# Performance work log

Measured on AMD Instinct MI355X. Metric: run time of the kernel, lower is better.

## Reference

```python
import math
import jax, jax.numpy as jnp
import numpy as np

B, T, G, E, H, L = 8, 32, 32, 768, 12, 4
S = T * G
HD = E // H


def setup_inputs() -> dict:
    key = jax.random.key(0)
    ks = jax.random.split(key, 10)
    def n(k, shape, s=0.02):
        return s * jax.random.normal(k, shape, jnp.float32)
    return dict(
        x=jax.random.normal(ks[0], (B, T, G, E), jnp.float32),
        study_date=jnp.sort(jax.random.randint(ks[1], (B, T), 0, 50), axis=-1),
        wpe=n(ks[2], (50, E)),
        ln1_w=jnp.ones((L, E)), ln1_b=jnp.zeros((L, E)),
        in_w=n(ks[3], (L, 3 * E, E)), in_b=jnp.zeros((L, 3 * E)),
        out_w=n(ks[4], (L, E, E)), out_b=jnp.zeros((L, E)),
        ln2_w=jnp.ones((L, E)), ln2_b=jnp.zeros((L, E)),
        fc_w=n(ks[5], (L, 4 * E, E)), fc_b=jnp.zeros((L, 4 * E)),
        proj_w=n(ks[6], (L, E, 4 * E), 0.02 / math.sqrt(2 * L)),
        proj_b=jnp.zeros((L, E)),
        lnf_w=jnp.ones((E,)), lnf_b=jnp.zeros((E,)),
    )


def _ln(x, w, b):
    m = x.mean(-1, keepdims=True)
    v = ((x - m) ** 2).mean(-1, keepdims=True)
    return (x - m) / jnp.sqrt(v + 1e-5) * w + b


def _gelu_new(x):
    # NewGELU: 0.5*x*(1+tanh(sqrt(2/pi)*(x+0.044715*x^3)))
    c = np.sqrt(2.0 / np.pi).astype(np.float32)
    return 0.5 * x * (1.0 + jnp.tanh(c * (x + 0.044715 * x ** 3)))


def _mask_bias():
    # block-causal mask: tril over T blocks, each expanded to G x G
    allowed = jnp.tril(jnp.ones((T, T), bool))
    allowed = jnp.repeat(jnp.repeat(allowed, G, axis=0), G, axis=1)  # [S,S]
    return jnp.where(allowed, 0.0, -jnp.inf).astype(jnp.float32)


def reference(x, study_date, wpe, ln1_w, ln1_b, in_w, in_b, out_w, out_b,
              ln2_w, ln2_b, fc_w, fc_b, proj_w, proj_b, lnf_w, lnf_b):
    b, t, g, d = x.shape
    s = t * g
    pos = wpe[jnp.clip(study_date, 0, 49)]  # [B,T,E]
    pos = jnp.broadcast_to(pos[:, :, None, :], (b, t, g, d)).reshape(b, s, d)
    h = x.reshape(b, s, d) + pos
    bias = _mask_bias()  # [S,S]
    inv_sqrt_hd = 1.0 / np.sqrt(HD).astype(np.float32)
    for l in range(L):
        y = _ln(h, ln1_w[l], ln1_b[l])
        qkv = y @ in_w[l].T + in_b[l]  # [B,S,3E]
        q, k, v = jnp.split(qkv, 3, axis=-1)
        q = q.reshape(b, s, H, HD).transpose(0, 2, 1, 3)
        k = k.reshape(b, s, H, HD).transpose(0, 2, 1, 3)
        v = v.reshape(b, s, H, HD).transpose(0, 2, 1, 3)
        att = jnp.einsum('bhqd,bhkd->bhqk', q, k) * inv_sqrt_hd + bias
        att = jax.nn.softmax(att, axis=-1)
        o = jnp.einsum('bhqk,bhkd->bhqd', att, v)
        o = o.transpose(0, 2, 1, 3).reshape(b, s, d)
        h = h + o @ out_w[l].T + out_b[l]
        y2 = _ln(h, ln2_w[l], ln2_b[l])
        h = h + _gelu_new(y2 @ fc_w[l].T + fc_b[l]) @ proj_w[l].T + proj_b[l]
    return _ln(h, lnf_w, lnf_b)
```

## Files before the change

### kernel.cpp

```cpp
#include <hip/hip_runtime.h>
#include <hip/hip_bf16.h>

typedef __attribute__((ext_vector_type(8))) __bf16 bf16x8;
typedef __attribute__((ext_vector_type(4))) float f32x4;

typedef unsigned short u16;

__device__ __forceinline__ u16 f2bf(float f) {
    unsigned int u = __float_as_uint(f);
    u += 0x7FFFu + ((u >> 16) & 1u);
    return (u16)(u >> 16);
}

__device__ __forceinline__ void g2l16(const void* g, void* l) {
    __builtin_amdgcn_global_load_lds(
        (const __attribute__((address_space(1))) void*)g,
        (__attribute__((address_space(3))) void*)l, 16, 0, 0);
}

#define BB 8
#define SS 1024
#define EE 768
#define HH 12
#define HD 64
#define LL 4

__global__ __launch_bounds__(256) void cvt_k(const float* __restrict__ in,
                                             u16* __restrict__ out, int n4) {
    for (int i = blockIdx.x * 256 + threadIdx.x; i < n4; i += gridDim.x * 256) {
        float4 v = ((const float4*)in)[i];
        ushort4 u;
        u.x = f2bf(v.x); u.y = f2bf(v.y); u.z = f2bf(v.z); u.w = f2bf(v.w);
        ((ushort4*)out)[i] = u;
    }
}

__global__ __launch_bounds__(256) void embed_k(const float* __restrict__ x,
                                               const int* __restrict__ sd,
                                               const float* __restrict__ wpe,
                                               float* __restrict__ h) {
    int idx = blockIdx.x * 256 + threadIdx.x;
    int e4 = idx % 192;
    int bs = idx / 192;
    int b = bs >> 10;
    int t = (bs >> 5) & 31;
    int date = sd[b * 32 + t];
    date = date < 0 ? 0 : (date > 49 ? 49 : date);
    float4 xv = ((const float4*)x)[idx];
    float4 pv = ((const float4*)wpe)[date * 192 + e4];
    float4 r; r.x = xv.x + pv.x; r.y = xv.y + pv.y; r.z = xv.z + pv.z; r.w = xv.w + pv.w;
    ((float4*)h)[idx] = r;
}

template <bool BF16OUT>
__global__ __launch_bounds__(256) void ln_k(const float* __restrict__ in,
                                            const float* __restrict__ w,
                                            const float* __restrict__ b,
                                            void* __restrict__ out) {
    int tid = threadIdx.x, wv = tid >> 6, lane = tid & 63;
    int token = blockIdx.x * 4 + wv;
    const float4* ip = (const float4*)(in + (size_t)token * EE);
    float4 v[3];
#pragma unroll
    for (int p = 0; p < 3; p++) v[p] = ip[p * 64 + lane];
    float s = 0.f;
#pragma unroll
    for (int p = 0; p < 3; p++) s += v[p].x + v[p].y + v[p].z + v[p].w;
#pragma unroll
    for (int m = 1; m < 64; m <<= 1) s += __shfl_xor(s, m);
    float mean = s * (1.f / 768.f);
    float vs = 0.f;
#pragma unroll
    for (int p = 0; p < 3; p++) {
        float dx = v[p].x - mean, dy = v[p].y - mean, dz = v[p].z - mean, dw = v[p].w - mean;
        vs += dx * dx + dy * dy + dz * dz + dw * dw;
    }
#pragma unroll
    for (int m = 1; m < 64; m <<= 1) vs += __shfl_xor(vs, m);
    float rstd = rsqrtf(vs * (1.f / 768.f) + 1e-5f);
    const float4* wp = (const float4*)w;
    const float4* bp = (const float4*)b;
#pragma unroll
    for (int p = 0; p < 3; p++) {
        float4 wv4 = wp[p * 64 + lane], bv4 = bp[p * 64 + lane];
        float rx = (v[p].x - mean) * rstd * wv4.x + bv4.x;
        float ry = (v[p].y - mean) * rstd * wv4.y + bv4.y;
        float rz = (v[p].z - mean) * rstd * wv4.z + bv4.z;
        float rw = (v[p].w - mean) * rstd * wv4.w + bv4.w;
        if (BF16OUT) {
            ushort4 u; u.x = f2bf(rx); u.y = f2bf(ry); u.z = f2bf(rz); u.w = f2bf(rw);
            ((ushort4*)((u16*)out + (size_t)token * EE))[p * 64 + lane] = u;
        } else {
            float4 r; r.x = rx; r.y = ry; r.z = rz; r.w = rw;
            ((float4*)((float*)out + (size_t)token * EE))[p * 64 + lane] = r;
        }
    }
}

template <int MODE, int BM>
__global__ __launch_bounds__(256) void gemm_bt(const u16* __restrict__ A,
                                               const u16* __restrict__ Bw,
                                               const float* __restrict__ bias,
                                               float* __restrict__ hres,
                                               u16* __restrict__ outb,
                                               u16* __restrict__ vT,
                                               u16* __restrict__ kT,
                                               int M, int N, int K) {
    constexpr int TM = BM / 32;
    constexpr int NST = (BM == 128) ? 3 : 4;
    constexpr int PD = NST - 2;
    constexpr int ATILE = BM * 32;
    constexpr int TILE = ATILE + 4096;
    constexpr int SSTR = TILE * 2;
    __shared__ u16 SM[NST * TILE];

    const int tid = threadIdx.x;
    const int lane = tid & 63, w = tid >> 6;
    const int quad = lane >> 4, l16 = lane & 15;

    const int nx = N >> 7;
    const int ny = M / BM;
    const int id = blockIdx.x;
    const int xcd = id & 7, s = id >> 3;
    const int yt = xcd * (ny >> 3) + s / nx;
    const int xt = s % nx;
    const int m0 = yt * BM, n0 = xt * 128;
    const int wm = (w >> 1) * (BM / 2), wn = (w & 1) * 64;

    f32x4 acc[TM][4];
#pragma unroll
    for (int i = 0; i < TM; i++)
#pragma unroll
        for (int j = 0; j < 4; j++) acc[i][j] = (f32x4){0.f, 0.f, 0.f, 0.f};

    const int swz = (quad ^ ((l16 >> 1) & 3)) * 8;
    const int nk = K >> 5;

    const int cB0 = w * 128 + lane, cB1 = cB0 + 64;
    const int rB0 = cB0 >> 2, gB0 = (((cB0 & 3) ^ ((cB0 >> 3) & 3)) * 8);
    const int rB1 = cB1 >> 2, gB1 = (((cB1 & 3) ^ ((cB1 >> 3) & 3)) * 8);
    const u16* Bp0 = Bw + (size_t)(n0 + rB0) * K + gB0;
    const u16* Bp1 = Bw + (size_t)(n0 + rB1) * K + gB1;
    char* lB0 = (char*)SM + ATILE * 2 + w * 2048;
    char* lB1 = lB0 + 1024;
    const int cA0 = (BM == 128) ? cB0 : tid;
    const int rA0 = cA0 >> 2, gA0 = (((cA0 & 3) ^ ((cA0 >> 3) & 3)) * 8);
    const u16* Ap0 = A + (size_t)(m0 + rA0) * K + gA0;
    char* lA0 = (char*)SM + ((BM == 128) ? w * 2048 : w * 1024);
    const int cA1 = cB1;
    const int rA1 = cA1 >> 2, gA1 = (((cA1 & 3) ^ ((cA1 >> 3) & 3)) * 8);
    const u16* Ap1 = A + (size_t)(m0 + rA1) * K + gA1;
    char* lA1 = (char*)SM + w * 2048 + 1024;

    g2l16(Ap0, lA0);
    if (BM == 128) g2l16(Ap1, lA1);
    g2l16(Bp0, lB0);
    g2l16(Bp1, lB1);
    if (PD == 2) {
        g2l16(Ap0 + 32, lA0 + SSTR);
        if (BM == 128) g2l16(Ap1 + 32, lA1 + SSTR);
        g2l16(Bp0 + 32, lB0 + SSTR);
        g2l16(Bp1 + 32, lB1 + SSTR);
    }

    int rb = 0, wb = PD;
    for (int ki = 0; ki < nk; ki++) {
        if (ki + PD < nk) {
            const int kb = (ki + PD) << 5;
            const int bo = wb * SSTR;
            g2l16(Ap0 + kb, lA0 + bo);
            if (BM == 128) g2l16(Ap1 + kb, lA1 + bo);
            g2l16(Bp0 + kb, lB0 + bo);
            g2l16(Bp1 + kb, lB1 + bo);
        }
        if (BM == 128) {
            if (ki < nk - 1) __builtin_amdgcn_s_waitcnt(0x0F74);
            else             __builtin_amdgcn_s_waitcnt(0x0F70);
        } else {
            if (ki < nk - 2)      __builtin_amdgcn_s_waitcnt(0x0F76);
            else if (ki == nk - 2) __builtin_amdgcn_s_waitcnt(0x0F73);
            else                  __builtin_amdgcn_s_waitcnt(0x0F70);
        }
        __builtin_amdgcn_s_barrier();

        const u16* Ab = (const u16*)SM + rb * TILE;
        const u16* Bb = Ab + ATILE;
        bf16x8 af[TM], bfr[4];
#pragma unroll
        for (int t = 0; t < TM; t++)
            af[t] = *(const bf16x8*)(Ab + (wm + t * 16 + l16) * 32 + swz);
#pragma unroll
        for (int t = 0; t < 4; t++)
            bfr[t] = *(const bf16x8*)(Bb + (wn + t * 16 + l16) * 32 + swz);
#pragma unroll
        for (int tm = 0; tm < TM; tm++)
#pragma unroll
            for (int tn = 0; tn < 4; tn++)
                acc[tm][tn] = __builtin_amdgcn_mfma_f32_16x16x32_bf16(
                    af[tm], bfr[tn], acc[tm][tn], 0, 0, 0);
        rb = (rb + 1 == NST) ? 0 : rb + 1;
        wb = (wb + 1 == NST) ? 0 : wb + 1;
    }

#pragma unroll
    for (int tm = 0; tm < TM; tm++) {
        int rowm = m0 + wm + tm * 16 + quad * 4;
#pragma unroll
        for (int tn = 0; tn < 4; tn++) {
            int coln = n0 + wn + tn * 16 + l16;
            float bv = bias[coln];
            f32x4 v = acc[tm][tn];
            if (MODE == 0) {
                int b = rowm >> 10, s2 = rowm & 1023;
                if (coln < EE) {
                    int hh = coln >> 6, d = coln & 63;
                    u16* qp = outb + ((size_t)(b * HH + hh) * SS + s2) * HD + d;
#pragma unroll
                    for (int r = 0; r < 4; r++) qp[r * HD] = f2bf(v[r] + bv);
                } else if (coln < 2 * EE) {
                    int hh = (coln - EE) >> 6, d = (coln - EE) & 63;
                    u16* kp = kT + ((size_t)(b * HH + hh) * SS + s2) * HD + d;
#pragma unroll
                    for (int r = 0; r < 4; r++) kp[r * HD] = f2bf(v[r] + bv);
                } else {
                    int hh = (coln - 2 * EE) >> 6, d = (coln - 2 * EE) & 63;
                    ushort4 pk;
                    pk.x = f2bf(v[0] + bv); pk.y = f2bf(v[1] + bv);
                    pk.z = f2bf(v[2] + bv); pk.w = f2bf(v[3] + bv);
                    *(ushort4*)(vT + (((size_t)((b * HH + hh) * HD + d)) << 10) + s2) = pk;
                }
            } else if (MODE == 1) {
#pragma unroll
                for (int r = 0; r < 4; r++) {
                    size_t idx = (size_t)(rowm + r) * N + coln;
                    hres[idx] += v[r] + bv;
                }
            } else {
#pragma unroll
                for (int r = 0; r < 4; r++) {
                    float x = v[r] + bv;
                    float t = x + 0.044715f * x * x * x;
                    float e = __expf(-1.5957691216057308f * t);
                    float th = (1.f - e) / (1.f + e);
                    outb[(size_t)(rowm + r) * N + coln] = f2bf(0.5f * x * (1.f + th));
                }
            }
        }
    }
}

__global__ __launch_bounds__(256) void attn_k(const u16* __restrict__ qT,
                                              const u16* __restrict__ kT,
                                              const u16* __restrict__ vT,
                                              u16* __restrict__ o) {
    __shared__ u16 Ks[2048];
    __shared__ u16 Vs[2048];
    __shared__ u16 P[4][16 * 40];
    int tid = threadIdx.x, w = tid >> 6, lane = tid & 63;
    int quad = lane >> 4, l16 = lane & 15;
    int blk = blockIdx.x;
    int qg = 15 - (blk / 96);
    int bh = blk % 96;
    int b = bh / HH, hh = bh % HH;
    int q0 = qg * 64;
    int kend_blk = q0 + 64;
    int kend_w = q0 + ((w >> 1) ? 64 : 32);

    const u16* qbase = qT + ((size_t)bh * SS + q0 + w * 16 + l16) * HD + quad * 8;
    bf16x8 qf0 = *(const bf16x8*)(qbase);
    bf16x8 qf1 = *(const bf16x8*)(qbase + 32);

    f32x4 of[4];
#pragma unroll
    for (int i = 0; i < 4; i++) of[i] = (f32x4){0.f, 0.f, 0.f, 0.f};
    float mrun[4], lrun[4];
#pragma unroll
    for (int r = 0; r < 4; r++) { mrun[r] = -__builtin_inff(); lrun[r] = 0.f; }

    int tK = tid >> 3, dcK = ((tid & 7) ^ (tK & 7));
    const u16* kg = kT + ((size_t)bh * SS + tK) * HD + dcK * 8;
    char* kl = (char*)Ks + w * 1024;
    int dV = tid >> 2, tcV = ((tid & 3) ^ ((dV >> 1) & 3));
    const u16* vg = vT + ((size_t)bh * HD + dV) * SS + tcV * 8;
    char* vl = (char*)Vs + w * 1024;
    u16* Pw = P[w];

    for (int kb = 0; kb < kend_blk; kb += 32) {
        g2l16(kg + (size_t)kb * HD, kl);
        g2l16(vg + kb, vl);
        __syncthreads();
        if (kb < kend_w) {
            int t0 = l16, t1 = 16 + l16;
            bf16x8 k00 = *(const bf16x8*)(Ks + (t0 * 8 + (quad ^ (l16 & 7))) * 8);
            bf16x8 k01 = *(const bf16x8*)(Ks + (t0 * 8 + ((4 + quad) ^ (l16 & 7))) * 8);
            bf16x8 k10 = *(const bf16x8*)(Ks + (t1 * 8 + (quad ^ (l16 & 7))) * 8);
            bf16x8 k11 = *(const bf16x8*)(Ks + (t1 * 8 + ((4 + quad) ^ (l16 & 7))) * 8);
            f32x4 s0 = (f32x4){0.f, 0.f, 0.f, 0.f};
            f32x4 s1 = (f32x4){0.f, 0.f, 0.f, 0.f};
            s0 = __builtin_amdgcn_mfma_f32_16x16x32_bf16(qf0, k00, s0, 0, 0, 0);
            s0 = __builtin_amdgcn_mfma_f32_16x16x32_bf16(qf1, k01, s0, 0, 0, 0);
            s1 = __builtin_amdgcn_mfma_f32_16x16x32_bf16(qf0, k10, s1, 0, 0, 0);
            s1 = __builtin_amdgcn_mfma_f32_16x16x32_bf16(qf1, k11, s1, 0, 0, 0);

            float alpha[4];
#pragma unroll
            for (int r = 0; r < 4; r++) {
                float a0 = s0[r] * 0.125f, a1 = s1[r] * 0.125f;
                float mx = fmaxf(a0, a1);
#pragma unroll
                for (int m = 1; m < 16; m <<= 1) mx = fmaxf(mx, __shfl_xor(mx, m));
                float mnew = fmaxf(mrun[r], mx);
                alpha[r] = __expf(mrun[r] - mnew);
                float p0 = __expf(a0 - mnew);
                float p1 = __expf(a1 - mnew);
                float ps = p0 + p1;
#pragma unroll
                for (int m = 1; m < 16; m <<= 1) ps += __shfl_xor(ps, m);
                lrun[r] = lrun[r] * alpha[r] + ps;
                mrun[r] = mnew;
                Pw[(quad * 4 + r) * 40 + l16] = f2bf(p0);
                Pw[(quad * 4 + r) * 40 + 16 + l16] = f2bf(p1);
            }
#pragma unroll
            for (int n4 = 0; n4 < 4; n4++) {
                of[n4][0] *= alpha[0]; of[n4][1] *= alpha[1];
                of[n4][2] *= alpha[2]; of[n4][3] *= alpha[3];
            }
            bf16x8 pf = *(const bf16x8*)(Pw + l16 * 40 + quad * 8);
#pragma unroll
            for (int n4 = 0; n4 < 4; n4++) {
                int d = n4 * 16 + l16;
                bf16x8 vf = *(const bf16x8*)(Vs + (d * 4 + (quad ^ ((d >> 1) & 3))) * 8);
                of[n4] = __builtin_amdgcn_mfma_f32_16x16x32_bf16(pf, vf, of[n4], 0, 0, 0);
            }
        }
        __syncthreads();
    }

    float inv[4];
#pragma unroll
    for (int r = 0; r < 4; r++) inv[r] = 1.f / lrun[r];
#pragma unroll
    for (int n4 = 0; n4 < 4; n4++)
#pragma unroll
        for (int r = 0; r < 4; r++)
            o[(size_t)(b * SS + q0 + w * 16 + quad * 4 + r) * EE + hh * HD + n4 * 16 + l16] =
                f2bf(of[n4][r] * inv[r]);
}

extern "C" void kernel_launch(void* const* d_in, const int* in_sizes, int n_in,
                              void* d_out, int out_size, void* d_ws, size_t ws_size,
                              hipStream_t stream) {
    const float* x     = (const float*)d_in[0];
    const int*   sd    = (const int*)d_in[1];
    const float* wpe   = (const float*)d_in[2];
    const float* ln1w  = (const float*)d_in[3];
    const float* ln1b  = (const float*)d_in[4];
    const float* in_w  = (const float*)d_in[5];
    const float* in_b  = (const float*)d_in[6];
    const float* out_w = (const float*)d_in[7];
    const float* out_b = (const float*)d_in[8];
    const float* ln2w  = (const float*)d_in[9];
    const float* ln2b  = (const float*)d_in[10];
    const float* fc_w  = (const float*)d_in[11];
    const float* fc_b  = (const float*)d_in[12];
    const float* pr_w  = (const float*)d_in[13];
    const float* pr_b  = (const float*)d_in[14];
    const float* lnfw  = (const float*)d_in[15];
    const float* lnfb  = (const float*)d_in[16];
    float* outp = (float*)d_out;

    char* ws = (char*)d_ws;
    float* h   = (float*)ws;
    u16* ybuf  = (u16*)(ws + 25165824);
    u16* big   = (u16*)(ws + 37748736);
    u16* qT    = big;
    u16* kT    = big + 6291456;
    u16* vT    = (u16*)(ws + 88080384);
    u16* wb    = (u16*)(ws + 100663296);
    u16* w_in  = wb;
    u16* w_out = w_in + 7077888;
    u16* w_fc  = w_out + 2359296;
    u16* w_pr  = w_fc + 9437184;

    cvt_k<<<1024, 256, 0, stream>>>(in_w,  w_in,  7077888 / 4);
    cvt_k<<<1024, 256, 0, stream>>>(out_w, w_out, 2359296 / 4);
    cvt_k<<<1024, 256, 0, stream>>>(fc_w,  w_fc,  9437184 / 4);
    cvt_k<<<1024, 256, 0, stream>>>(pr_w,  w_pr,  9437184 / 4);
    embed_k<<<6144, 256, 0, stream>>>(x, sd, wpe, h);

    for (int l = 0; l < LL; l++) {
        ln_k<true><<<2048, 256, 0, stream>>>(h, ln1w + l * EE, ln1b + l * EE, ybuf);
        gemm_bt<0, 128><<<18 * 64, 256, 0, stream>>>(
            ybuf, w_in + (size_t)l * 2304 * 768, in_b + l * 2304, nullptr, qT, vT, kT,
            8192, 2304, 768);
        attn_k<<<1536, 256, 0, stream>>>(qT, kT, vT, ybuf);
        gemm_bt<1, 64><<<6 * 128, 256, 0, stream>>>(
            ybuf, w_out + (size_t)l * 768 * 768, out_b + l * 768, h, nullptr, nullptr, nullptr,
            8192, 768, 768);
        ln_k<true><<<2048, 256, 0, stream>>>(h, ln2w + l * EE, ln2b + l * EE, ybuf);
        gemm_bt<2, 128><<<24 * 64, 256, 0, stream>>>(
            ybuf, w_fc + (size_t)l * 3072 * 768, fc_b + l * 3072, nullptr, big, nullptr, nullptr,
            8192, 3072, 768);
        gemm_bt<1, 64><<<6 * 128, 256, 0, stream>>>(
            big, w_pr + (size_t)l * 768 * 3072, pr_b + l * 768, h, nullptr, nullptr, nullptr,
            8192, 768, 3072);
    }
    ln_k<false><<<2048, 256, 0, stream>>>(h, lnfw, lnfb, outp);
}
```

Measured before the change: 1.294 ms.

## Add register-staged B-operand GEMM for residual out-proj and MLP-proj

Adds a new GEMM kernel for the two residual-add projections. Only the A tile is staged through LDS, with a 4-stage ring and async global-to-LDS loads. Each wave loads its B (weight) fragments straight from global memory into a 3-deep register ring, with explicit vmcnt waits. This is meant to cut LDS traffic and bank pressure for the weight operand and to overlap loads with MFMA, at the cost of more registers and uncoalesced per-lane global loads of B. The kernel also uses XCD-aware block swizzling.

```diff
diff --git a/kernel.cpp b/kernel.cpp
--- a/kernel.cpp
+++ b/kernel.cpp
@@ -244,6 +244,104 @@
                     float th = (1.f - e) / (1.f + e);
                     outb[(size_t)(rowm + r) * N + coln] = f2bf(0.5f * x * (1.f + th));
                 }
+            }
+        }
+    }
+}
+
+__global__ __launch_bounds__(256, 3) void gemm_breg(const u16* __restrict__ A,
+                                                    const u16* __restrict__ Bw,
+                                                    const float* __restrict__ bias,
+                                                    float* __restrict__ hres,
+                                                    int M, int N, int K) {
+    constexpr int NST = 4;
+    __shared__ u16 SM[NST * 2048];
+
+    const int tid = threadIdx.x;
+    const int lane = tid & 63, w = tid >> 6;
+    const int quad = lane >> 4, l16 = lane & 15;
+
+    const int nx = N >> 7;
+    const int ny = M >> 6;
+    const int id = blockIdx.x;
+    const int xcd = id & 7, s = id >> 3;
+    const int yt = xcd * (ny >> 3) + s / nx;
+    const int xt = s % nx;
+    const int m0 = yt * 64, n0 = xt * 128;
+    const int wm = (w >> 1) * 32, wn = (w & 1) * 64;
+
+    f32x4 acc[2][4];
+#pragma unroll
+    for (int i = 0; i < 2; i++)
+#pragma unroll
+        for (int j = 0; j < 4; j++) acc[i][j] = (f32x4){0.f, 0.f, 0.f, 0.f};
+
+    const int swz = (quad ^ ((l16 >> 1) & 3)) * 8;
+    const int nk = K >> 5;
+
+    const int rA0 = tid >> 2, gA0 = (((tid & 3) ^ ((tid >> 3) & 3)) * 8);
+    const u16* Ap0 = A + (size_t)(m0 + rA0) * K + gA0;
+    char* lA0 = (char*)SM + w * 1024;
+
+    const u16* BpR[4];
+#pragma unroll
+    for (int t = 0; t < 4; t++)
+        BpR[t] = Bw + (size_t)(n0 + wn + t * 16 + l16) * K + quad * 8;
+
+    bf16x8 bb0[4], bb1[4], bb2[4];
+
+    g2l16(Ap0, lA0);
+#pragma unroll
+    for (int t = 0; t < 4; t++) bb0[t] = *(const bf16x8*)(BpR[t]);
+    g2l16(Ap0 + 32, lA0 + 4096);
+#pragma unroll
+    for (int t = 0; t < 4; t++) bb1[t] = *(const bf16x8*)(BpR[t] + 32);
+
+    int rb = 0;
+    for (int ki0 = 0; ki0 < nk; ki0 += 3) {
+#pragma unroll
+        for (int j = 0; j < 3; j++) {
+            const int ki = ki0 + j;
+            if (ki + 2 < nk) {
+                const int kb = (ki + 2) << 5;
+                g2l16(Ap0 + kb, lA0 + (size_t)((rb + 2) & 3) * 4096);
+                bf16x8* bw = (j == 0) ? bb2 : (j == 1) ? bb0 : bb1;
+#pragma unroll
+                for (int t = 0; t < 4; t++) bw[t] = *(const bf16x8*)(BpR[t] + kb);
+            }
+            const int rem = nk - 1 - ki;
+            if (rem >= 2)      asm volatile("s_waitcnt vmcnt(10)" ::: "memory");
+            else if (rem == 1) asm volatile("s_waitcnt vmcnt(5)" ::: "memory");
+            else               asm volatile("s_waitcnt vmcnt(0)" ::: "memory");
+            __builtin_amdgcn_s_barrier();
+
+            const u16* Ab = (const u16*)SM + rb * 2048;
+            bf16x8 af0 = *(const bf16x8*)(Ab + (wm + l16) * 32 + swz);
+            bf16x8 af1 = *(const bf16x8*)(Ab + (wm + 16 + l16) * 32 + swz);
+            const bf16x8* br = (j == 0) ? bb0 : (j == 1) ? bb1 : bb2;
+#pragma unroll
+            for (int tn = 0; tn < 4; tn++) {
+                acc[0][tn] = __builtin_amdgcn_mfma_f32_16x16x32_bf16(
+                    af0, br[tn], acc[0][tn], 0, 0, 0);
+                acc[1][tn] = __builtin_amdgcn_mfma_f32_16x16x32_bf16(
+                    af1, br[tn], acc[1][tn], 0, 0, 0);
+            }
+            rb = (rb + 1) & 3;
+        }
+    }
+
+#pragma unroll
+    for (int tm = 0; tm < 2; tm++) {
+        int rowm = m0 + wm + tm * 16 + quad * 4;
+#pragma unroll
+        for (int tn = 0; tn < 4; tn++) {
+            int coln = n0 + wn + tn * 16 + l16;
+            float bv = bias[coln];
+            f32x4 v = acc[tm][tn];
+#pragma unroll
+            for (int r = 0; r < 4; r++) {
+                size_t idx = (size_t)(rowm + r) * N + coln;
+                hres[idx] += v[r] + bv;
             }
         }
     }
@@ -395,15 +493,15 @@
             ybuf, w_in + (size_t)l * 2304 * 768, in_b + l * 2304, nullptr, qT, vT, kT,
             8192, 2304, 768);
         attn_k<<<1536, 256, 0, stream>>>(qT, kT, vT, ybuf);
-        gemm_bt<1, 64><<<6 * 128, 256, 0, stream>>>(
-            ybuf, w_out + (size_t)l * 768 * 768, out_b + l * 768, h, nullptr, nullptr, nullptr,
+        gemm_breg<<<6 * 128, 256, 0, stream>>>(
+            ybuf, w_out + (size_t)l * 768 * 768, out_b + l * 768, h,
             8192, 768, 768);
         ln_k<true><<<2048, 256, 0, stream>>>(h, ln2w + l * EE, ln2b + l * EE, ybuf);
         gemm_bt<2, 128><<<24 * 64, 256, 0, stream>>>(
             ybuf, w_fc + (size_t)l * 3072 * 768, fc_b + l * 3072, nullptr, big, nullptr, nullptr,
             8192, 3072, 768);
-        gemm_bt<1, 64><<<6 * 128, 256, 0, stream>>>(
-            big, w_pr + (size_t)l * 768 * 3072, pr_b + l * 768, h, nullptr, nullptr, nullptr,
+        gemm_breg<<<6 * 128, 256, 0, stream>>>(
+            big, w_pr + (size_t)l * 768 * 3072, pr_b + l * 768, h,
             8192, 768, 3072);
     }
     ln_k<false><<<2048, 256, 0, stream>>>(h, lnfw, lnfb, outp);
```

Result: slower. 1.672 ms (+29.2%).
